# Kernel tuning notes

Measured on AMD Instinct MI355X. Metric: run time of the kernel, lower is better.

## Reference

```python
import jax, jax.numpy as jnp
import numpy as np
from jax import lax

X_SIZE, Z_SIZE, H, GC, PD = 256, 64, 64, 16, 2
B, K, T = 256, 16, 50
LOG_SIG_MIN, LOG_SIG_MAX, LOG_P_MAX = -10.0, 10.0, 50.0
ZX = X_SIZE + Z_SIZE
LSTM_IN = ZX + PD


def setup_inputs() -> dict:
    key = jax.random.key(0)
    ks = jax.random.split(key, 24)
    s = lambda fan_in: 1.0 / np.sqrt(fan_in)
    u = lambda k, shape, sc: jax.random.uniform(k, shape, jnp.float32, -sc, sc)
    inp = {
        'x': jax.random.normal(ks[0], (B, X_SIZE), jnp.float32),
        'z_stacked': jax.random.normal(ks[1], (K, B, Z_SIZE), jnp.float32),
        'input_seqs': jax.random.normal(ks[2], (B, 8, 2, 2, 6), jnp.float32),
        'pred_seqs': jax.random.normal(ks[3], (B, T, 2, 2, 6), jnp.float32),
        # initial_h / initial_c linears: ZX -> H
        'Wh0': u(ks[4], (H, ZX), s(ZX)), 'bh0': u(ks[5], (H,), s(ZX)),
        'Wc0': u(ks[6], (H, ZX), s(ZX)), 'bc0': u(ks[7], (H,), s(ZX)),
        # LSTMCell: gates order i,f,g,o
        'Wih': u(ks[8], (4 * H, LSTM_IN), s(H)), 'Whh': u(ks[9], (4 * H, H), s(H)),
        'bih': u(ks[10], (4 * H,), s(H)), 'bhh': u(ks[11], (4 * H,), s(H)),
        # GMM parameter heads: H -> GC / GC*PD
        'Wpi': u(ks[12], (GC, H), s(H)), 'bpi': u(ks[13], (GC,), s(H)),
        'Wmu': u(ks[14], (GC * PD, H), s(H)), 'bmu': u(ks[15], (GC * PD,), s(H)),
        'Wls': u(ks[16], (GC * PD, H), s(H)), 'bls': u(ks[17], (GC * PD,), s(H)),
        'Wcorr': u(ks[18], (GC, H), s(H)), 'bcorr': u(ks[19], (GC,), s(H)),
        'n_z_samples': K,
    }
    return inp


def _gmm2d_log_prob(log_pis, mus, log_sigmas, corrs, value):
    # log_pis/corrs: [K,B,T,GC]; mus/log_sigmas: [K,B,T,GC*PD]; value: [B,T,PD]
    ls = jnp.clip(log_sigmas, LOG_SIG_MIN, LOG_SIG_MAX).reshape(K, B, T, GC, PD)
    mu = mus.reshape(K, B, T, GC, PD)
    dx = value[None, :, :, None, :] - mu                      # [K,B,T,GC,PD]
    zscore = dx * jnp.exp(-ls)                                # dx / sigma
    one_m_rho2 = 1.0 - corrs ** 2
    quad = (zscore[..., 0] ** 2 + zscore[..., 1] ** 2
            - 2.0 * corrs * zscore[..., 0] * zscore[..., 1])
    comp = (-jnp.log(2.0 * jnp.pi) - ls.sum(-1)
            - 0.5 * jnp.log(one_m_rho2) - 0.5 * quad / one_m_rho2)
    log_pi_n = jax.nn.log_softmax(log_pis, axis=-1)
    log_p_t = jax.nn.logsumexp(log_pi_n + comp, axis=-1)      # [K,B,T]
    return jnp.minimum(log_p_t, LOG_P_MAX)


def reference(x, z_stacked, input_seqs, pred_seqs,
              Wh0, bh0, Wc0, bc0, Wih, Whh, bih, bhh,
              Wpi, bpi, Wmu, bmu, Wls, bls, Wcorr, bcorr, n_z_samples):
    tgt_future = pred_seqs[:, :, 1, 1, 2:4]                   # [B,T,2]
    tgt_present = input_seqs[:, -1, 1, 1, 2:4]                # [B,2]
    z = z_stacked.reshape(-1, z_stacked.shape[-1])            # [K*B, z]
    zx = jnp.concatenate([z, jnp.tile(x, (n_z_samples, 1))], axis=1)  # [N, ZX]
    N = zx.shape[0]
    h0 = zx @ Wh0.T + bh0
    c0 = zx @ Wc0.T + bc0
    decode_inputs = jnp.concatenate([tgt_present[:, None, :], tgt_future[:, :T - 1, :]], axis=1)  # [B,T,2]
    inputs = jnp.concatenate([
        jnp.broadcast_to(zx[:, None, :], (N, T, ZX)),
        jnp.tile(decode_inputs, (n_z_samples, 1, 1))], axis=2)  # [N,T,ZX+2]

    def step(carry, xt):
        h, c = carry
        gates = xt @ Wih.T + bih + h @ Whh.T + bhh
        i, f, g, o = jnp.split(gates, 4, axis=-1)
        c = jax.nn.sigmoid(f) * c + jax.nn.sigmoid(i) * jnp.tanh(g)
        h = jax.nn.sigmoid(o) * jnp.tanh(c)
        return (h, c), h

    _, hs = lax.scan(step, (h0, c0), jnp.swapaxes(inputs, 0, 1))  # [T,N,H]
    hs = jnp.swapaxes(hs, 0, 1)                                   # [N,T,H]

    log_pis = (hs @ Wpi.T + bpi).reshape(K, B, T, GC)
    mus = (hs @ Wmu.T + bmu).reshape(K, B, T, GC * PD)
    log_sigmas = (hs @ Wls.T + bls).reshape(K, B, T, GC * PD)
    corrs = jnp.tanh(hs @ Wcorr.T + bcorr).reshape(K, B, T, GC)

    log_p_yt_xz = _gmm2d_log_prob(log_pis, mus, log_sigmas, corrs, tgt_future)
    return log_p_yt_xz.sum(axis=2)                                # [K,B]
```

## Files before the change

### kernel.cpp

```cpp
#include <hip/hip_runtime.h>


#define T_ 50
typedef __attribute__((ext_vector_type(8))) short short8;
typedef __attribute__((ext_vector_type(4))) float f32x4;
#define MFMA(a,b,c) __builtin_amdgcn_mfma_f32_16x16x32_bf16(a,b,c,0,0,0)

__device__ __forceinline__ float sigf(float x)  { return 1.0f / (1.0f + __expf(-x)); }
__device__ __forceinline__ float tanh_(float x) { return 1.0f - 2.0f / (__expf(2.0f * x) + 1.0f); }

__device__ __forceinline__ void splitf(float f, unsigned short& hi, unsigned short& lo) {
    unsigned b = __float_as_uint(f);
    hi = (unsigned short)(b >> 16);
    float fh = __uint_as_float(b & 0xffff0000u);
    lo = (unsigned short)(__float_as_uint(f - fh) >> 16);
}

__device__ __forceinline__ void pack8(const float* p, short8& hi, short8& lo) {
    #pragma unroll
    for (int e = 0; e < 8; ++e) {
        unsigned short h, l;
        splitf(p[e], h, l);
        hi[e] = (short)h; lo[e] = (short)l;
    }
}

__launch_bounds__(768, 3)
__global__ void decoder_kernel(
    const float* __restrict__ x,       const float* __restrict__ z,
    const float* __restrict__ inp_seqs,const float* __restrict__ pred_seqs,
    const float* __restrict__ Wh0,     const float* __restrict__ bh0,
    const float* __restrict__ Wc0,     const float* __restrict__ bc0,
    const float* __restrict__ Wih,     const float* __restrict__ Whh,
    const float* __restrict__ bih,     const float* __restrict__ bhh,
    const float* __restrict__ Wpi,     const float* __restrict__ bpi,
    const float* __restrict__ Wmu,     const float* __restrict__ bmu,
    const float* __restrict__ Wls,     const float* __restrict__ bls,
    const float* __restrict__ Wcorr,   const float* __restrict__ bcorr,
    float* __restrict__ out)
{
    __shared__ __align__(16) float smem[7488];
    float* ZXL = smem;
    float* gcX = smem;
    float* c0X = smem + 4096;
    float* PL0 = smem;
    float* PL1 = smem + 1600;
    float* FUT = smem + 3200;
    float* PRS = smem + 4800;
    unsigned short* HF0h = (unsigned short*)(smem + 5184);
    unsigned short* HF0l = HF0h + 1152;
    unsigned short* HF1h = HF0h + 2304;
    unsigned short* HF1l = HF0h + 3456;

    const int j = threadIdx.x;
    const int w = j >> 6;
    const int l = j & 63;
    const int g = l >> 4;
    const int c = l & 15;
    const int blk = blockIdx.x;

    for (int e = j; e < 16*320; e += 768) {
        int s = e / 320, k = e - s*320;
        int n = blk*16 + s, b = n & 255;
        ZXL[s*324 + k] = (k < 64) ? z[n*64 + k] : x[b*256 + (k - 64)];
    }
    __syncthreads();

    const int tA = w;
    f32x4 accA, accB;
    const float* srcA;
    const float* srcB;
    int tB = -1;
    {
        int qA_ = tA >> 2, ubA_ = tA & 3;
        int gaA = qA_*64 + 16*ubA_ + c;
        float bA = bih[gaA] + bhh[gaA];
        accA = (f32x4){bA, bA, bA, bA};
        srcA = Wih + gaA*322;
        float bB;
        if (w < 4) {
            tB = 12 + w;
            int qB_ = tB >> 2, ubB_ = tB & 3;
            int gaB = qB_*64 + 16*ubB_ + c;
            bB = bih[gaB] + bhh[gaB];
            srcB = Wih + gaB*322;
        } else if (w < 8) {
            int u = 16*(w-4) + c;
            bB = bh0[u];
            srcB = Wh0 + u*320;
        } else {
            int u = 16*(w-8) + c;
            bB = bc0[u];
            srcB = Wc0 + u*320;
        }
        accB = (f32x4){bB, bB, bB, bB};
    }
    for (int ks = 0; ks < 10; ++ks) {
        short8 ah, al;
        pack8(&ZXL[c*324 + ks*32 + g*8], ah, al);
        short8 b1h, b1l; pack8(srcA + ks*32 + g*8, b1h, b1l);
        accA = MFMA(ah, b1h, accA); accA = MFMA(ah, b1l, accA); accA = MFMA(al, b1h, accA);
        short8 b2h, b2l; pack8(srcB + ks*32 + g*8, b2h, b2l);
        accB = MFMA(ah, b2h, accB); accB = MFMA(ah, b2l, accB); accB = MFMA(al, b2h, accB);
    }
    __syncthreads();

    #pragma unroll
    for (int r = 0; r < 4; ++r) gcX[tA*256 + (4*g + r)*16 + c] = accA[r];
    if (w < 4) {
        #pragma unroll
        for (int r = 0; r < 4; ++r) gcX[tB*256 + (4*g + r)*16 + c] = accB[r];
    } else if (w < 8) {
        #pragma unroll
        for (int r = 0; r < 4; ++r) {
            unsigned short hh, ll; splitf(accB[r], hh, ll);
            HF0h[(4*g + r)*72 + 16*(w-4) + c] = hh;
            HF0l[(4*g + r)*72 + 16*(w-4) + c] = ll;
        }
    } else {
        #pragma unroll
        for (int r = 0; r < 4; ++r) c0X[(4*g + r)*64 + 16*(w-8) + c] = accB[r];
    }
    __syncthreads();

    f32x4 gc[4];
    float cst[4];
    short8 WH[4][2], WL[4][2];
    float wd0[4], wd1[4];
    short8 qAh0, qAl0, qAh1, qAl1, qBh0, qBl0, qBh1, qBl1;
    float pbA = 0.0f, pbB = 0.0f;
    int ptA = 0, nproj = 0;
    const int s3 = 4*(w - 8) + g;
    const int g3 = c;
    float sum = 0.0f;

    if (w < 4) {
        #pragma unroll
        for (int q = 0; q < 4; ++q) {
            #pragma unroll
            for (int r = 0; r < 4; ++r)
                gc[q][r] = gcX[(q*4 + w)*256 + (4*g + r)*16 + c];
            int ga = q*64 + 16*w + c;
            pack8(Whh + ga*64 +      g*8, WH[q][0], WL[q][0]);
            pack8(Whh + ga*64 + 32 + g*8, WH[q][1], WL[q][1]);
            wd0[q] = Wih[ga*322 + 320];
            wd1[q] = Wih[ga*322 + 321];
        }
        #pragma unroll
        for (int r = 0; r < 4; ++r) cst[r] = c0X[(4*g + r)*64 + 16*w + c];
    } else if (w < 8) {
        int v = w - 4;
        nproj = (v < 2) ? 2 : 1;
        ptA = (v < 2) ? 2*v : 4 + (v - 2);
        auto projrow = [&](int r3, const float*& p, float& b) {
            if      (r3 < 16) { p = Wpi   + r3*64;      b = bpi[r3]; }
            else if (r3 < 48) { p = Wmu   + (r3-16)*64; b = bmu[r3-16]; }
            else if (r3 < 80) { p = Wls   + (r3-48)*64; b = bls[r3-48]; }
            else              { p = Wcorr + (r3-80)*64; b = bcorr[r3-80]; }
        };
        const float* p;
        projrow(ptA*16 + c, p, pbA);
        pack8(p +      g*8, qAh0, qAl0);
        pack8(p + 32 + g*8, qAh1, qAl1);
        if (nproj == 2) {
            projrow((ptA+1)*16 + c, p, pbB);
            pack8(p +      g*8, qBh0, qBl0);
            pack8(p + 32 + g*8, qBh1, qBl1);
        }
    }
    __syncthreads();

    for (int e = j; e < T_*32; e += 768) {
        int t = e >> 5, rem = e & 31, s = rem >> 1;
        int b = (blk*16 + s) & 255;
        FUT[e] = pred_seqs[b*1200 + t*24 + 20 + (rem & 1)];
    }
    if (j < 32) {
        int b = (blk*16 + (j >> 1)) & 255;
        PRS[j] = inp_seqs[b*192 + 188 + (j & 1)];
    }
    __syncthreads();

    auto do_proj = [&](const unsigned short* Hh, const unsigned short* Hl, float* PLw) {
        short8 ah0 = *reinterpret_cast<const short8*>(Hh + c*72 +      g*8);
        short8 al0 = *reinterpret_cast<const short8*>(Hl + c*72 +      g*8);
        short8 ah1 = *reinterpret_cast<const short8*>(Hh + c*72 + 32 + g*8);
        short8 al1 = *reinterpret_cast<const short8*>(Hl + c*72 + 32 + g*8);
        f32x4 pA = (f32x4){pbA, pbA, pbA, pbA};
        pA = MFMA(ah0, qAh0, pA); pA = MFMA(ah0, qAl0, pA); pA = MFMA(al0, qAh0, pA);
        pA = MFMA(ah1, qAh1, pA); pA = MFMA(ah1, qAl1, pA); pA = MFMA(al1, qAh1, pA);
        #pragma unroll
        for (int r = 0; r < 4; ++r) PLw[(4*g + r)*100 + ptA*16 + c] = pA[r];
        if (nproj == 2) {
            f32x4 pB = (f32x4){pbB, pbB, pbB, pbB};
            pB = MFMA(ah0, qBh0, pB); pB = MFMA(ah0, qBl0, pB); pB = MFMA(al0, qBh0, pB);
            pB = MFMA(ah1, qBh1, pB); pB = MFMA(ah1, qBl1, pB); pB = MFMA(al1, qBh1, pB);
            #pragma unroll
            for (int r = 0; r < 4; ++r) PLw[(4*g + r)*100 + (ptA+1)*16 + c] = pB[r];
        }
    };
    auto do_gmm = [&](const float* pl, const float* fut2) {
        const float* pls = pl + s3*100;
        float a_pi = pls[g3];
        float a_m0 = pls[16 + 2*g3], a_m1 = pls[17 + 2*g3];
        float l0   = pls[48 + 2*g3], l1   = pls[49 + 2*g3];
        float a_co = pls[80 + g3];
        float v0 = fut2[s3*2], v1 = fut2[s3*2 + 1];
        l0 = fminf(fmaxf(l0, -10.0f), 10.0f);
        l1 = fminf(fmaxf(l1, -10.0f), 10.0f);
        float z0 = (v0 - a_m0) * __expf(-l0);
        float z1 = (v1 - a_m1) * __expf(-l1);
        float ct = tanh_(a_co);
        float omr = 1.0f - ct*ct;
        float quad = z0*z0 + z1*z1 - 2.0f*ct*z0*z1;
        float comp = -1.8378770664093453f - (l0 + l1) - 0.5f*__logf(omr) - 0.5f*quad/omr;
        float a = a_pi + comp;
        float m1v = a, m2v = a_pi;
        #pragma unroll
        for (int off = 1; off < 16; off <<= 1) {
            m1v = fmaxf(m1v, __shfl_xor(m1v, off));
            m2v = fmaxf(m2v, __shfl_xor(m2v, off));
        }
        float e1 = __expf(a - m1v), e2 = __expf(a_pi - m2v);
        #pragma unroll
        for (int off = 1; off < 16; off <<= 1) {
            e1 += __shfl_xor(e1, off);
            e2 += __shfl_xor(e2, off);
        }
        float logp = (m1v + __logf(e1)) - (m2v + __logf(e2));
        sum += fminf(logp, 50.0f);
    };

    for (int t = 0; t < T_; ++t) {
        const unsigned short* Hh = (t & 1) ? HF1h : HF0h;
        const unsigned short* Hl = (t & 1) ? HF1l : HF0l;
        if (w < 4) {
            unsigned short* Nh = (t & 1) ? HF0h : HF1h;
            unsigned short* Nl = (t & 1) ? HF0l : HF1l;
            short8 ah0 = *reinterpret_cast<const short8*>(Hh + c*72 +      g*8);
            short8 al0 = *reinterpret_cast<const short8*>(Hl + c*72 +      g*8);
            short8 ah1 = *reinterpret_cast<const short8*>(Hh + c*72 + 32 + g*8);
            short8 al1 = *reinterpret_cast<const short8*>(Hl + c*72 + 32 + g*8);
            const float* dptr = (t == 0) ? PRS : (FUT + (t-1)*32);
            float2 dv[4];
            #pragma unroll
            for (int r = 0; r < 4; ++r)
                dv[r] = *reinterpret_cast<const float2*>(dptr + (4*g + r)*2);
            f32x4 aq[4];
            #pragma unroll
            for (int q = 0; q < 4; ++q) {
                #pragma unroll
                for (int r = 0; r < 4; ++r)
                    aq[q][r] = gc[q][r] + dv[r].x*wd0[q] + dv[r].y*wd1[q];
                aq[q] = MFMA(ah0, WH[q][0], aq[q]);
                aq[q] = MFMA(ah0, WL[q][0], aq[q]);
                aq[q] = MFMA(al0, WH[q][0], aq[q]);
                aq[q] = MFMA(ah1, WH[q][1], aq[q]);
                aq[q] = MFMA(ah1, WL[q][1], aq[q]);
                aq[q] = MFMA(al1, WH[q][1], aq[q]);
            }
            #pragma unroll
            for (int r = 0; r < 4; ++r) {
                float cc = sigf(aq[1][r])*cst[r] + sigf(aq[0][r])*tanh_(aq[2][r]);
                cst[r] = cc;
                float hv = sigf(aq[3][r])*tanh_(cc);
                unsigned short hh, ll; splitf(hv, hh, ll);
                Nh[(4*g + r)*72 + 16*w + c] = hh;
                Nl[(4*g + r)*72 + 16*w + c] = ll;
            }
        } else if (w < 8) {
            if (t >= 1) do_proj(Hh, Hl, (t & 1) ? PL1 : PL0);
        } else {
            if (t >= 2) do_gmm((t & 1) ? PL0 : PL1, FUT + (t-2)*32);
        }
        __syncthreads();
    }

    if (w >= 4 && w < 8) do_proj(HF0h, HF0l, PL0);
    if (w >= 8) do_gmm(PL1, FUT + 48*32);
    __syncthreads();
    if (w >= 8) {
        do_gmm(PL0, FUT + 49*32);
        if (g3 == 0) out[blk*16 + s3] = sum;
    }
}

extern "C" void kernel_launch(void* const* d_in, const int* in_sizes, int n_in,
                              void* d_out, int out_size, void* d_ws, size_t ws_size,
                              hipStream_t stream) {
    const float* x     = (const float*)d_in[0];
    const float* z     = (const float*)d_in[1];
    const float* iseq  = (const float*)d_in[2];
    const float* pseq  = (const float*)d_in[3];
    const float* Wh0   = (const float*)d_in[4];
    const float* bh0   = (const float*)d_in[5];
    const float* Wc0   = (const float*)d_in[6];
    const float* bc0   = (const float*)d_in[7];
    const float* Wih   = (const float*)d_in[8];
    const float* Whh   = (const float*)d_in[9];
    const float* bih   = (const float*)d_in[10];
    const float* bhh   = (const float*)d_in[11];
    const float* Wpi   = (const float*)d_in[12];
    const float* bpi   = (const float*)d_in[13];
    const float* Wmu   = (const float*)d_in[14];
    const float* bmu   = (const float*)d_in[15];
    const float* Wls   = (const float*)d_in[16];
    const float* bls   = (const float*)d_in[17];
    const float* Wcorr = (const float*)d_in[18];
    const float* bcorr = (const float*)d_in[19];
    float* out = (float*)d_out;

    decoder_kernel<<<256, 768, 0, stream>>>(x, z, iseq, pseq, Wh0, bh0, Wc0, bc0,
                                            Wih, Whh, bih, bhh, Wpi, bpi, Wmu, bmu,
                                            Wls, bls, Wcorr, bcorr, out);
}
```

Before: 98.50 us.

## Split decoder into 512 blocks of 8 sequences with bf16 weights in LDS

Each block now handles 8 sequences instead of 16 across 8 waves, and the grid doubles to 512 blocks. Sequences are placed on alternate MFMA rows, so half of each accumulator is padding. Whh and the projection weights become single round-to-nearest bf16 values staged in LDS rather than hi/lo split pairs held in registers, which cuts the MFMA count per gate from 6 to 4 at some cost in accuracy. The LSTM waves also raise their scheduling priority during the recurrent step, all to shorten the serial per-timestep critical path and spread work over more CUs.

```diff
diff --git a/kernel.cpp b/kernel.cpp
--- a/kernel.cpp
+++ b/kernel.cpp
@@ -15,7 +15,6 @@
     float fh = __uint_as_float(b & 0xffff0000u);
     lo = (unsigned short)(__float_as_uint(f - fh) >> 16);
 }
-
 __device__ __forceinline__ void pack8(const float* p, short8& hi, short8& lo) {
     #pragma unroll
     for (int e = 0; e < 8; ++e) {
@@ -24,8 +23,17 @@
         hi[e] = (short)h; lo[e] = (short)l;
     }
 }
-
-__launch_bounds__(768, 3)
+__device__ __forceinline__ unsigned short bf16rn(float f) {
+    unsigned b = __float_as_uint(f);
+    unsigned r = b + 0x7fffu + ((b >> 16) & 1u);
+    return (unsigned short)(r >> 16);
+}
+__device__ __forceinline__ void pack8rn(const float* p, short8& hi) {
+    #pragma unroll
+    for (int e = 0; e < 8; ++e) hi[e] = (short)bf16rn(p[e]);
+}
+
+__launch_bounds__(512, 4)
 __global__ void decoder_kernel(
     const float* __restrict__ x,       const float* __restrict__ z,
     const float* __restrict__ inp_seqs,const float* __restrict__ pred_seqs,
@@ -39,18 +47,19 @@
     const float* __restrict__ Wcorr,   const float* __restrict__ bcorr,
     float* __restrict__ out)
 {
-    __shared__ __align__(16) float smem[7488];
-    float* ZXL = smem;
-    float* gcX = smem;
-    float* c0X = smem + 4096;
-    float* PL0 = smem;
-    float* PL1 = smem + 1600;
-    float* FUT = smem + 3200;
-    float* PRS = smem + 4800;
-    unsigned short* HF0h = (unsigned short*)(smem + 5184);
-    unsigned short* HF0l = HF0h + 1152;
-    unsigned short* HF1h = HF0h + 2304;
-    unsigned short* HF1l = HF0h + 3456;
+    __shared__ __align__(16) float smem[18752];
+    short8* WHH = (short8*)smem;
+    short8* PRJ = (short8*)(smem + 8192);
+    unsigned short* HF0h = (unsigned short*)(smem + 11264);
+    unsigned short* HF0l = (unsigned short*)(smem + 11840);
+    unsigned short* HF1h = (unsigned short*)(smem + 12416);
+    unsigned short* HF1l = (unsigned short*)(smem + 12992);
+    float* C0X = smem + 12416;
+    float* ZXL = smem + 13568;
+    float* PL0 = smem + 13568;
+    float* PL1 = smem + 15168;
+    float* FUT = smem + 16768;
+    float* PRS = smem + 17568;
 
     const int j = threadIdx.x;
     const int w = j >> 6;
@@ -59,152 +68,122 @@
     const int c = l & 15;
     const int blk = blockIdx.x;
 
-    for (int e = j; e < 16*320; e += 768) {
+    for (int e = j; e < 5184; e += 512) ZXL[e] = 0.0f;
+    for (int e = j; e < 1152; e += 512) smem[11264 + e] = 0.0f;
+    __syncthreads();
+
+    for (int e = j; e < 8*320; e += 512) {
         int s = e / 320, k = e - s*320;
-        int n = blk*16 + s, b = n & 255;
-        ZXL[s*324 + k] = (k < 64) ? z[n*64 + k] : x[b*256 + (k - 64)];
-    }
-    __syncthreads();
-
-    const int tA = w;
-    f32x4 accA, accB;
-    const float* srcA;
-    const float* srcB;
-    int tB = -1;
-    {
-        int qA_ = tA >> 2, ubA_ = tA & 3;
-        int gaA = qA_*64 + 16*ubA_ + c;
-        float bA = bih[gaA] + bhh[gaA];
-        accA = (f32x4){bA, bA, bA, bA};
-        srcA = Wih + gaA*322;
-        float bB;
-        if (w < 4) {
-            tB = 12 + w;
-            int qB_ = tB >> 2, ubB_ = tB & 3;
-            int gaB = qB_*64 + 16*ubB_ + c;
-            bB = bih[gaB] + bhh[gaB];
-            srcB = Wih + gaB*322;
-        } else if (w < 8) {
-            int u = 16*(w-4) + c;
-            bB = bh0[u];
-            srcB = Wh0 + u*320;
+        int n = blk*8 + s, b = n & 255;
+        ZXL[(2*s)*324 + k] = (k < 64) ? z[n*64 + k] : x[b*256 + (k - 64)];
+    }
+    for (int e = j; e < 2816; e += 512) {
+        int lane = e & 63, slot = e >> 6;
+        int gg = lane >> 4, cc = lane & 15;
+        short8 hi;
+        if (slot < 32) {
+            int ks = slot & 1, tile = slot >> 1;
+            int q = tile >> 2, ub = tile & 3;
+            pack8rn(Whh + (q*64 + 16*ub + cc)*64 + ks*32 + gg*8, hi);
+            WHH[slot*64 + lane] = hi;
         } else {
-            int u = 16*(w-8) + c;
-            bB = bc0[u];
-            srcB = Wc0 + u*320;
-        }
-        accB = (f32x4){bB, bB, bB, bB};
-    }
-    for (int ks = 0; ks < 10; ++ks) {
-        short8 ah, al;
-        pack8(&ZXL[c*324 + ks*32 + g*8], ah, al);
-        short8 b1h, b1l; pack8(srcA + ks*32 + g*8, b1h, b1l);
-        accA = MFMA(ah, b1h, accA); accA = MFMA(ah, b1l, accA); accA = MFMA(al, b1h, accA);
-        short8 b2h, b2l; pack8(srcB + ks*32 + g*8, b2h, b2l);
-        accB = MFMA(ah, b2h, accB); accB = MFMA(ah, b2l, accB); accB = MFMA(al, b2h, accB);
-    }
-    __syncthreads();
-
-    #pragma unroll
-    for (int r = 0; r < 4; ++r) gcX[tA*256 + (4*g + r)*16 + c] = accA[r];
+            int s2 = slot - 32;
+            int ks = s2 & 1, pt = s2 >> 1;
+            int r3 = pt*16 + cc;
+            const float* p;
+            if      (r3 < 16) p = Wpi   + r3*64;
+            else if (r3 < 48) p = Wmu   + (r3-16)*64;
+            else if (r3 < 80) p = Wls   + (r3-48)*64;
+            else              p = Wcorr + (r3-80)*64;
+            pack8rn(p + ks*32 + gg*8, hi);
+            PRJ[s2*64 + lane] = hi;
+        }
+    }
+    __syncthreads();
+
+    float gc0v[4], gc1v[4], wd0[4], wd1[4];
+    float cst0 = 0.0f, cst1 = 0.0f;
+    float biasP[3] = {0.0f, 0.0f, 0.0f};
+    float sum = 0.0f;
+    const int s3 = 4*(w - 6) + g;
+
     if (w < 4) {
-        #pragma unroll
-        for (int r = 0; r < 4; ++r) gcX[tB*256 + (4*g + r)*16 + c] = accB[r];
-    } else if (w < 8) {
-        #pragma unroll
-        for (int r = 0; r < 4; ++r) {
-            unsigned short hh, ll; splitf(accB[r], hh, ll);
-            HF0h[(4*g + r)*72 + 16*(w-4) + c] = hh;
-            HF0l[(4*g + r)*72 + 16*(w-4) + c] = ll;
-        }
-    } else {
-        #pragma unroll
-        for (int r = 0; r < 4; ++r) c0X[(4*g + r)*64 + 16*(w-8) + c] = accB[r];
-    }
-    __syncthreads();
-
-    f32x4 gc[4];
-    float cst[4];
-    short8 WH[4][2], WL[4][2];
-    float wd0[4], wd1[4];
-    short8 qAh0, qAl0, qAh1, qAl1, qBh0, qBl0, qBh1, qBl1;
-    float pbA = 0.0f, pbB = 0.0f;
-    int ptA = 0, nproj = 0;
-    const int s3 = 4*(w - 8) + g;
-    const int g3 = c;
-    float sum = 0.0f;
-
-    if (w < 4) {
+        f32x4 gcA[4];
         #pragma unroll
         for (int q = 0; q < 4; ++q) {
-            #pragma unroll
-            for (int r = 0; r < 4; ++r)
-                gc[q][r] = gcX[(q*4 + w)*256 + (4*g + r)*16 + c];
             int ga = q*64 + 16*w + c;
-            pack8(Whh + ga*64 +      g*8, WH[q][0], WL[q][0]);
-            pack8(Whh + ga*64 + 32 + g*8, WH[q][1], WL[q][1]);
+            float b_ = bih[ga] + bhh[ga];
+            gcA[q] = (f32x4){b_, 0.0f, b_, 0.0f};
             wd0[q] = Wih[ga*322 + 320];
             wd1[q] = Wih[ga*322 + 321];
         }
-        #pragma unroll
-        for (int r = 0; r < 4; ++r) cst[r] = c0X[(4*g + r)*64 + 16*w + c];
-    } else if (w < 8) {
-        int v = w - 4;
-        nproj = (v < 2) ? 2 : 1;
-        ptA = (v < 2) ? 2*v : 4 + (v - 2);
-        auto projrow = [&](int r3, const float*& p, float& b) {
-            if      (r3 < 16) { p = Wpi   + r3*64;      b = bpi[r3]; }
-            else if (r3 < 48) { p = Wmu   + (r3-16)*64; b = bmu[r3-16]; }
-            else if (r3 < 80) { p = Wls   + (r3-48)*64; b = bls[r3-48]; }
-            else              { p = Wcorr + (r3-80)*64; b = bcorr[r3-80]; }
-        };
-        const float* p;
-        projrow(ptA*16 + c, p, pbA);
-        pack8(p +      g*8, qAh0, qAl0);
-        pack8(p + 32 + g*8, qAh1, qAl1);
-        if (nproj == 2) {
-            projrow((ptA+1)*16 + c, p, pbB);
-            pack8(p +      g*8, qBh0, qBl0);
-            pack8(p + 32 + g*8, qBh1, qBl1);
-        }
-    }
-    __syncthreads();
-
-    for (int e = j; e < T_*32; e += 768) {
-        int t = e >> 5, rem = e & 31, s = rem >> 1;
-        int b = (blk*16 + s) & 255;
+        for (int ks = 0; ks < 10; ++ks) {
+            short8 ah, al;
+            pack8(&ZXL[c*324 + ks*32 + g*8], ah, al);
+            #pragma unroll
+            for (int q = 0; q < 4; ++q) {
+                int ga = q*64 + 16*w + c;
+                short8 bh_, bl_;
+                pack8(Wih + ga*322 + ks*32 + g*8, bh_, bl_);
+                gcA[q] = MFMA(ah, bh_, gcA[q]);
+                gcA[q] = MFMA(ah, bl_, gcA[q]);
+                gcA[q] = MFMA(al, bh_, gcA[q]);
+            }
+        }
+        #pragma unroll
+        for (int q = 0; q < 4; ++q) { gc0v[q] = gcA[q][0]; gc1v[q] = gcA[q][2]; }
+    } else {
+        int v = w - 4, u = 16*v + c;
+        float bhv = bh0[u], bcv = bc0[u];
+        f32x4 h0a = (f32x4){bhv, 0.0f, bhv, 0.0f};
+        f32x4 c0a = (f32x4){bcv, 0.0f, bcv, 0.0f};
+        for (int ks = 0; ks < 10; ++ks) {
+            short8 ah, al, bh_, bl_, ch_, cl_;
+            pack8(&ZXL[c*324 + ks*32 + g*8], ah, al);
+            pack8(Wh0 + u*320 + ks*32 + g*8, bh_, bl_);
+            pack8(Wc0 + u*320 + ks*32 + g*8, ch_, cl_);
+            h0a = MFMA(ah, bh_, h0a); h0a = MFMA(ah, bl_, h0a); h0a = MFMA(al, bh_, h0a);
+            c0a = MFMA(ah, ch_, c0a); c0a = MFMA(ah, cl_, c0a); c0a = MFMA(al, ch_, c0a);
+        }
+        unsigned short hh, ll;
+        splitf(h0a[0], hh, ll); HF0h[(4*g)*72 + u] = hh;   HF0l[(4*g)*72 + u] = ll;
+        splitf(h0a[2], hh, ll); HF0h[(4*g+2)*72 + u] = hh; HF0l[(4*g+2)*72 + u] = ll;
+        C0X[(2*g)*64 + u]   = c0a[0];
+        C0X[(2*g+1)*64 + u] = c0a[2];
+    }
+    __syncthreads();
+
+    if (w < 4) {
+        cst0 = C0X[(2*g)*64 + 16*w + c];
+        cst1 = C0X[(2*g+1)*64 + 16*w + c];
+    } else if (w < 6) {
+        #pragma unroll
+        for (int i = 0; i < 3; ++i) {
+            int r3 = (3*(w-4) + i)*16 + c;
+            biasP[i] = (r3 < 16) ? bpi[r3] : (r3 < 48) ? bmu[r3-16]
+                     : (r3 < 80) ? bls[r3-48] : bcorr[r3-80];
+        }
+    }
+    __syncthreads();
+
+    for (int e = j; e < 1152; e += 512) smem[12416 + e] = 0.0f;
+    for (int e = j; e < T_*16; e += 512) {
+        int t = e >> 4, rem = e & 15, s = rem >> 1;
+        int b = (blk*8 + s) & 255;
         FUT[e] = pred_seqs[b*1200 + t*24 + 20 + (rem & 1)];
     }
-    if (j < 32) {
-        int b = (blk*16 + (j >> 1)) & 255;
+    if (j < 16) {
+        int b = (blk*8 + (j >> 1)) & 255;
         PRS[j] = inp_seqs[b*192 + 188 + (j & 1)];
     }
     __syncthreads();
 
-    auto do_proj = [&](const unsigned short* Hh, const unsigned short* Hl, float* PLw) {
-        short8 ah0 = *reinterpret_cast<const short8*>(Hh + c*72 +      g*8);
-        short8 al0 = *reinterpret_cast<const short8*>(Hl + c*72 +      g*8);
-        short8 ah1 = *reinterpret_cast<const short8*>(Hh + c*72 + 32 + g*8);
-        short8 al1 = *reinterpret_cast<const short8*>(Hl + c*72 + 32 + g*8);
-        f32x4 pA = (f32x4){pbA, pbA, pbA, pbA};
-        pA = MFMA(ah0, qAh0, pA); pA = MFMA(ah0, qAl0, pA); pA = MFMA(al0, qAh0, pA);
-        pA = MFMA(ah1, qAh1, pA); pA = MFMA(ah1, qAl1, pA); pA = MFMA(al1, qAh1, pA);
-        #pragma unroll
-        for (int r = 0; r < 4; ++r) PLw[(4*g + r)*100 + ptA*16 + c] = pA[r];
-        if (nproj == 2) {
-            f32x4 pB = (f32x4){pbB, pbB, pbB, pbB};
-            pB = MFMA(ah0, qBh0, pB); pB = MFMA(ah0, qBl0, pB); pB = MFMA(al0, qBh0, pB);
-            pB = MFMA(ah1, qBh1, pB); pB = MFMA(ah1, qBl1, pB); pB = MFMA(al1, qBh1, pB);
-            #pragma unroll
-            for (int r = 0; r < 4; ++r) PLw[(4*g + r)*100 + (ptA+1)*16 + c] = pB[r];
-        }
-    };
     auto do_gmm = [&](const float* pl, const float* fut2) {
-        const float* pls = pl + s3*100;
-        float a_pi = pls[g3];
-        float a_m0 = pls[16 + 2*g3], a_m1 = pls[17 + 2*g3];
-        float l0   = pls[48 + 2*g3], l1   = pls[49 + 2*g3];
-        float a_co = pls[80 + g3];
+        const float* pls = pl + (2*s3)*100;
+        float a_pi = pls[c];
+        float a_m0 = pls[16 + 2*c], a_m1 = pls[17 + 2*c];
+        float l0   = pls[48 + 2*c], l1   = pls[49 + 2*c];
+        float a_co = pls[80 + c];
         float v0 = fut2[s3*2], v1 = fut2[s3*2 + 1];
         l0 = fminf(fmaxf(l0, -10.0f), 10.0f);
         l1 = fminf(fmaxf(l1, -10.0f), 10.0f);
@@ -230,6 +209,23 @@
         float logp = (m1v + __logf(e1)) - (m2v + __logf(e2));
         sum += fminf(logp, 50.0f);
     };
+    auto do_proj = [&](const unsigned short* Hh, const unsigned short* Hl, float* PLw) {
+        short8 ah0 = *reinterpret_cast<const short8*>(Hh + c*72 +      g*8);
+        short8 al0 = *reinterpret_cast<const short8*>(Hl + c*72 +      g*8);
+        short8 ah1 = *reinterpret_cast<const short8*>(Hh + c*72 + 32 + g*8);
+        short8 al1 = *reinterpret_cast<const short8*>(Hl + c*72 + 32 + g*8);
+        #pragma unroll
+        for (int i = 0; i < 3; ++i) {
+            int pt = 3*(w-4) + i;
+            short8 B0 = PRJ[(pt*2 + 0)*64 + l];
+            short8 B1 = PRJ[(pt*2 + 1)*64 + l];
+            f32x4 p = (f32x4){biasP[i], biasP[i], biasP[i], biasP[i]};
+            p = MFMA(ah0, B0, p); p = MFMA(al0, B0, p);
+            p = MFMA(ah1, B1, p); p = MFMA(al1, B1, p);
+            PLw[(4*g)*100 + pt*16 + c]   = p[0];
+            PLw[(4*g+2)*100 + pt*16 + c] = p[2];
+        }
+    };
 
     for (int t = 0; t < T_; ++t) {
         const unsigned short* Hh = (t & 1) ? HF1h : HF0h;
@@ -241,47 +237,51 @@
             short8 al0 = *reinterpret_cast<const short8*>(Hl + c*72 +      g*8);
             short8 ah1 = *reinterpret_cast<const short8*>(Hh + c*72 + 32 + g*8);
             short8 al1 = *reinterpret_cast<const short8*>(Hl + c*72 + 32 + g*8);
-            const float* dptr = (t == 0) ? PRS : (FUT + (t-1)*32);
-            float2 dv[4];
-            #pragma unroll
-            for (int r = 0; r < 4; ++r)
-                dv[r] = *reinterpret_cast<const float2*>(dptr + (4*g + r)*2);
+            const float* dptr = (t == 0) ? PRS : (FUT + (t-1)*16);
+            float2 d0 = *reinterpret_cast<const float2*>(dptr + 4*g);
+            float2 d1 = *reinterpret_cast<const float2*>(dptr + 4*g + 2);
+            __builtin_amdgcn_s_setprio(1);
             f32x4 aq[4];
             #pragma unroll
             for (int q = 0; q < 4; ++q) {
-                #pragma unroll
-                for (int r = 0; r < 4; ++r)
-                    aq[q][r] = gc[q][r] + dv[r].x*wd0[q] + dv[r].y*wd1[q];
-                aq[q] = MFMA(ah0, WH[q][0], aq[q]);
-                aq[q] = MFMA(ah0, WL[q][0], aq[q]);
-                aq[q] = MFMA(al0, WH[q][0], aq[q]);
-                aq[q] = MFMA(ah1, WH[q][1], aq[q]);
-                aq[q] = MFMA(ah1, WL[q][1], aq[q]);
-                aq[q] = MFMA(al1, WH[q][1], aq[q]);
+                f32x4 a;
+                a[0] = gc0v[q] + d0.x*wd0[q] + d0.y*wd1[q];
+                a[1] = 0.0f;
+                a[2] = gc1v[q] + d1.x*wd0[q] + d1.y*wd1[q];
+                a[3] = 0.0f;
+                short8 B0 = WHH[((q*4 + w)*2 + 0)*64 + l];
+                short8 B1 = WHH[((q*4 + w)*2 + 1)*64 + l];
+                a = MFMA(ah0, B0, a);
+                a = MFMA(al0, B0, a);
+                a = MFMA(ah1, B1, a);
+                a = MFMA(al1, B1, a);
+                aq[q] = a;
             }
-            #pragma unroll
-            for (int r = 0; r < 4; ++r) {
-                float cc = sigf(aq[1][r])*cst[r] + sigf(aq[0][r])*tanh_(aq[2][r]);
-                cst[r] = cc;
-                float hv = sigf(aq[3][r])*tanh_(cc);
-                unsigned short hh, ll; splitf(hv, hh, ll);
-                Nh[(4*g + r)*72 + 16*w + c] = hh;
-                Nl[(4*g + r)*72 + 16*w + c] = ll;
-            }
-        } else if (w < 8) {
+            float cc0 = sigf(aq[1][0])*cst0 + sigf(aq[0][0])*tanh_(aq[2][0]);
+            float cc1 = sigf(aq[1][2])*cst1 + sigf(aq[0][2])*tanh_(aq[2][2]);
+            cst0 = cc0; cst1 = cc1;
+            float hv0 = sigf(aq[3][0])*tanh_(cc0);
+            float hv1 = sigf(aq[3][2])*tanh_(cc1);
+            __builtin_amdgcn_s_setprio(0);
+            unsigned short hh, ll;
+            splitf(hv0, hh, ll);
+            Nh[(4*g)*72 + 16*w + c] = hh;   Nl[(4*g)*72 + 16*w + c] = ll;
+            splitf(hv1, hh, ll);
+            Nh[(4*g+2)*72 + 16*w + c] = hh; Nl[(4*g+2)*72 + 16*w + c] = ll;
+        } else if (w < 6) {
             if (t >= 1) do_proj(Hh, Hl, (t & 1) ? PL1 : PL0);
         } else {
-            if (t >= 2) do_gmm((t & 1) ? PL0 : PL1, FUT + (t-2)*32);
+            if (t >= 2) do_gmm((t & 1) ? PL0 : PL1, FUT + (t-2)*16);
         }
         __syncthreads();
     }
 
-    if (w >= 4 && w < 8) do_proj(HF0h, HF0l, PL0);
-    if (w >= 8) do_gmm(PL1, FUT + 48*32);
-    __syncthreads();
-    if (w >= 8) {
-        do_gmm(PL0, FUT + 49*32);
-        if (g3 == 0) out[blk*16 + s3] = sum;
+    if (w == 4 || w == 5) do_proj(HF0h, HF0l, PL0);
+    if (w >= 6) do_gmm(PL1, FUT + 48*16);
+    __syncthreads();
+    if (w >= 6) {
+        do_gmm(PL0, FUT + 49*16);
+        if (c == 0) out[blk*8 + s3] = sum;
     }
 }
 
@@ -310,7 +310,7 @@
     const float* bcorr = (const float*)d_in[19];
     float* out = (float*)d_out;
 
-    decoder_kernel<<<256, 768, 0, stream>>>(x, z, iseq, pseq, Wh0, bh0, Wc0, bc0,
+    decoder_kernel<<<512, 512, 0, stream>>>(x, z, iseq, pseq, Wh0, bh0, Wc0, bc0,
                                             Wih, Whh, bih, bhh, Wpi, bpi, Wmu, bmu,
                                             Wls, bls, Wcorr, bcorr, out);
 }
```

Measured after the change: 113.5 us. 15.2% more time.
